# Optimization experiments

Measured on AMD Instinct MI355X. Metric: run time of the kernel, lower is better.

## Reference

```python
import jax, jax.numpy as jnp
import numpy as np

B, S, D, H = 2, 2048, 1024, 16
HD = D // H


def setup_inputs() -> dict:
    key = jax.random.key(0)
    ks = jax.random.split(key, 9)
    x = jax.random.normal(ks[0], (B, S, D), dtype=jnp.float32)
    scale = 1.0 / np.sqrt(D)
    Wq = jax.random.normal(ks[1], (D, D), dtype=jnp.float32) * scale
    bq = jnp.zeros((D,), dtype=jnp.float32)
    Wk = jax.random.normal(ks[2], (D, D), dtype=jnp.float32) * scale
    bk = jnp.zeros((D,), dtype=jnp.float32)
    Wv = jax.random.normal(ks[3], (D, D), dtype=jnp.float32) * scale
    bv = jnp.zeros((D,), dtype=jnp.float32)
    Wo = jax.random.normal(ks[4], (D, D), dtype=jnp.float32) * scale
    bo = jnp.zeros((D,), dtype=jnp.float32)
    return {"x": x, "Wq": Wq, "bq": bq, "Wk": Wk, "bk": bk,
            "Wv": Wv, "bv": bv, "Wo": Wo, "bo": bo}


def reference(x, Wq, bq, Wk, bk, Wv, bv, Wo, bo):
    b, s, d = x.shape
    h, hd = H, HD
    # torch Linear: y = x @ W.T + b
    q = (x @ Wq.T + bq).reshape(b, s, h, hd).transpose(0, 2, 1, 3)  # (b,h,s,hd)
    k = (x @ Wk.T + bk).reshape(b, s, h, hd).transpose(0, 2, 1, 3)
    v = (x @ Wv.T + bv).reshape(b, s, h, hd).transpose(0, 2, 1, 3)
    scores = jnp.einsum('bhqd,bhkd->bhqk', q, k) / np.sqrt(hd)  # (b,h,s,s)
    # FAITHFUL to source: softmax over dim=1 (head axis), not the key axis.
    attn = jax.nn.softmax(scores, axis=1)
    # dropout is identity at inference
    out = jnp.einsum('bhqk,bhkd->bhqd', attn, v)  # (b,h,s,hd)
    out = out.transpose(0, 2, 1, 3).reshape(b, s, d)
    return out @ Wo.T + bo
```

## Files before the change

### kernel.cpp

```cpp
#include <hip/hip_runtime.h>
#include <hip/hip_bf16.h>
#include <cstdint>
#include <cstddef>


typedef __bf16 bf16x8 __attribute__((ext_vector_type(8)));
typedef __bf16 bf16x4 __attribute__((ext_vector_type(4)));
typedef _Float16 f16x2 __attribute__((ext_vector_type(2)));
typedef _Float16 f16x4 __attribute__((ext_vector_type(4)));
typedef _Float16 f16x8 __attribute__((ext_vector_type(8)));
typedef float floatx4 __attribute__((ext_vector_type(4)));

#define S_LEN 2048
#define DIM 1024
#define NH 16
#define HD 64
#define MTOT 4096
#define C_EXP 0.1803368801111244f

__device__ __forceinline__ float fast_exp2(float x) { return __builtin_amdgcn_exp2f(x); }

__device__ __forceinline__ f16x2 pk_cvt(float a, float b) {
    return __builtin_bit_cast(f16x2, __builtin_amdgcn_cvt_pkrtz(a, b));
}

__device__ __forceinline__ void g2l16(const void* g, void* l) {
    __builtin_amdgcn_global_load_lds(
        (const __attribute__((address_space(1))) void*)g,
        (__attribute__((address_space(3))) void*)l, 16, 0, 0);
}

__global__ void cast_all(const float* __restrict__ x,
                         const float* __restrict__ w0, const float* __restrict__ w1,
                         const float* __restrict__ w2, const float* __restrict__ w3,
                         __bf16* __restrict__ xb,
                         __bf16* __restrict__ o0, __bf16* __restrict__ o1,
                         __bf16* __restrict__ o2, _Float16* __restrict__ o3) {
    int bid = blockIdx.x;
    if (bid < 4096) {
        int i = (bid * 256 + threadIdx.x) * 4;
        float4 v = *(const float4*)&x[i];
        bf16x4 o;
        o.x = (__bf16)v.x; o.y = (__bf16)v.y; o.z = (__bf16)v.z; o.w = (__bf16)v.w;
        *(bf16x4*)&xb[i] = o;
        return;
    }
    bid -= 4096;
    int wi = bid >> 10;
    int i = ((bid & 1023) * 256 + threadIdx.x) * 4;
    if (wi == 3) {
        float4 v = *(const float4*)&w3[i];
        f16x4 o;
        o[0] = (_Float16)v.x; o[1] = (_Float16)v.y; o[2] = (_Float16)v.z; o[3] = (_Float16)v.w;
        *(f16x4*)&o3[i] = o;
        return;
    }
    const float* s = (wi == 0) ? w0 : (wi == 1) ? w1 : w2;
    __bf16* d = (wi == 0) ? o0 : (wi == 1) ? o1 : o2;
    float4 v = *(const float4*)&s[i];
    bf16x4 o;
    o.x = (__bf16)v.x; o.y = (__bf16)v.y; o.z = (__bf16)v.z; o.w = (__bf16)v.w;
    *(bf16x4*)&d[i] = o;
}

__global__ __launch_bounds__(256, 2) void qkv_gemm(const __bf16* __restrict__ A,
                                                   const __bf16* __restrict__ Wq,
                                                   const __bf16* __restrict__ Wk,
                                                   const __bf16* __restrict__ Wv,
                                                   const float* __restrict__ bq,
                                                   const float* __restrict__ bk,
                                                   const float* __restrict__ bv,
                                                   __bf16* __restrict__ Qo,
                                                   __bf16* __restrict__ Ko,
                                                   _Float16* __restrict__ Vt) {
    const int tng = blockIdx.x * 128, tm = blockIdx.y * 128;
    const int wsel = tng >> 10, tn = tng & 1023;
    const __bf16* W = (wsel == 0) ? Wq : (wsel == 1) ? Wk : Wv;
    const float* bias = (wsel == 0) ? bq : (wsel == 1) ? bk : bv;
    __shared__ __bf16 As[128 * 32];
    __shared__ __bf16 Bs[128 * 32];
    const int tid = threadIdx.x, wid = tid >> 6, lane = tid & 63;
    const int l15 = lane & 15, quad = lane >> 4;
    const int wm = (wid >> 1) * 64, wn = (wid & 1) * 64;
    floatx4 acc[4][4] = {};
    for (int k0 = 0; k0 < DIM; k0 += 32) {
        __syncthreads();
#pragma unroll
        for (int i = 0; i < 2; ++i) {
            int slot = i * 256 + tid;
            int r = slot >> 2, c8 = (slot & 3) * 8;
            g2l16(&A[(size_t)(tm + r) * DIM + k0 + c8], &As[slot * 8]);
            g2l16(&W[(size_t)(tn + r) * DIM + k0 + c8], &Bs[slot * 8]);
        }
        __syncthreads();
        bf16x8 af[4], bf[4];
#pragma unroll
        for (int t = 0; t < 4; ++t) {
            af[t] = *(const bf16x8*)&As[(wm + t * 16 + l15) * 32 + quad * 8];
            bf[t] = *(const bf16x8*)&Bs[(wn + t * 16 + l15) * 32 + quad * 8];
        }
#pragma unroll
        for (int im = 0; im < 4; ++im)
#pragma unroll
            for (int in = 0; in < 4; ++in)
                acc[im][in] = __builtin_amdgcn_mfma_f32_16x16x32_bf16(af[im], bf[in], acc[im][in], 0, 0, 0);
    }
    if (wsel < 2) {
        __bf16* O = wsel ? Ko : Qo;
#pragma unroll
        for (int im = 0; im < 4; ++im)
#pragma unroll
            for (int in = 0; in < 4; ++in)
#pragma unroll
                for (int r = 0; r < 4; ++r) {
                    int row = tm + wm + im * 16 + quad * 4 + r;
                    int col = tn + wn + in * 16 + l15;
                    O[(size_t)row * DIM + col] = (__bf16)(acc[im][in][r] + bias[col]);
                }
    } else {
#pragma unroll
        for (int im = 0; im < 4; ++im)
#pragma unroll
            for (int in = 0; in < 4; ++in) {
                int cv = tn + wn + in * 16 + l15;
                int row4 = tm + wm + im * 16 + quad * 4;
                float bv_ = bias[cv];
                f16x4 o;
#pragma unroll
                for (int r = 0; r < 4; ++r) o[r] = (_Float16)(acc[im][in][r] + bv_);
                *(f16x4*)&Vt[(size_t)cv * MTOT + row4] = o;
            }
    }
}

__global__ __launch_bounds__(512, 8) void den8(const __bf16* __restrict__ Q,
                                               const __bf16* __restrict__ Km,
                                               _Float16* __restrict__ rd) {
    const int kt = blockIdx.x * 64, qt = blockIdx.y * 128, b = blockIdx.z;
    __shared__ __bf16 Ks[2][2 * 2 * 64 * 32];
    const int tid = threadIdx.x, wid = tid >> 6, lane = tid & 63;
    const int l15 = lane & 15, quad = lane >> 4;
    const int kswz = ((lane >> 1) & 3) << 3;
    const int wq = wid * 16;
    floatx4 dsum[4] = {};
    const size_t qrow = (size_t)(b * S_LEN + qt + wq + l15) * DIM;
    const size_t kbase = (size_t)(b * S_LEN + kt) * DIM;

#pragma unroll
    for (int i = 0; i < 2; ++i) {
        int slot = i * 512 + tid;
        int hs = slot >> 9, rem = slot & 511;
        int p = rem >> 8, rem2 = rem & 255;
        int r = rem2 >> 2;
        int c8 = (((rem2 & 3) ^ ((rem2 >> 3) & 3)) * 8);
        g2l16(&Km[kbase + (size_t)r * DIM + hs * HD + p * 32 + c8], &Ks[0][slot * 8]);
    }
    for (int hh = 0; hh < 8; ++hh) {
        const int cur = hh & 1, nxt = cur ^ 1;
        __syncthreads();
        bf16x8 af[2][2];
#pragma unroll
        for (int hs = 0; hs < 2; ++hs) {
            af[hs][0] = *(const bf16x8*)&Q[qrow + (hh * 2 + hs) * HD + quad * 8];
            af[hs][1] = *(const bf16x8*)&Q[qrow + (hh * 2 + hs) * HD + 32 + quad * 8];
        }
        if (hh + 1 < 8) {
#pragma unroll
            for (int i = 0; i < 2; ++i) {
                int slot = i * 512 + tid;
                int hs = slot >> 9, rem = slot & 511;
                int p = rem >> 8, rem2 = rem & 255;
                int r = rem2 >> 2;
                int c8 = (((rem2 & 3) ^ ((rem2 >> 3) & 3)) * 8);
                g2l16(&Km[kbase + (size_t)r * DIM + ((hh + 1) * 2 + hs) * HD + p * 32 + c8],
                      &Ks[nxt][slot * 8]);
            }
        }
#pragma unroll
        for (int hs = 0; hs < 2; ++hs) {
#pragma unroll
            for (int n = 0; n < 4; ++n) {
                bf16x8 b0 = *(const bf16x8*)&Ks[cur][hs * 4096 + (n * 16 + l15) * 32 + ((quad * 8) ^ kswz)];
                bf16x8 b1 = *(const bf16x8*)&Ks[cur][hs * 4096 + 2048 + (n * 16 + l15) * 32 + ((quad * 8) ^ kswz)];
                floatx4 acc = {};
                acc = __builtin_amdgcn_mfma_f32_16x16x32_bf16(af[hs][0], b0, acc, 0, 0, 0);
                acc = __builtin_amdgcn_mfma_f32_16x16x32_bf16(af[hs][1], b1, acc, 0, 0, 0);
                floatx4 sc = acc * C_EXP;
                floatx4 e;
#pragma unroll
                for (int r = 0; r < 4; ++r) e[r] = fast_exp2(sc[r]);
                dsum[n] += e;
            }
        }
    }
#pragma unroll
    for (int n = 0; n < 4; ++n)
#pragma unroll
        for (int r = 0; r < 4; ++r) {
            int q = qt + wq + quad * 4 + r;
            int k = kt + n * 16 + l15;
            rd[(size_t)(b * S_LEN + q) * S_LEN + k] = (_Float16)(1.0f / dsum[n][r]);
        }
}

__global__ __launch_bounds__(512, 8) void attn8(const __bf16* __restrict__ Q,
                                                const __bf16* __restrict__ Km,
                                                const _Float16* __restrict__ Vt,
                                                const _Float16* __restrict__ rd,
                                                _Float16* __restrict__ AO1,
                                                _Float16* __restrict__ AO2) {
    const int qt = (blockIdx.x >> 1) * 128, ks = blockIdx.x & 1;
    const int h = blockIdx.y, b = blockIdx.z;
    __shared__ __bf16 Ks[2][2 * 64 * 32];
    __shared__ _Float16 Vts[2][64 * 72];
    const int tid = threadIdx.x, wid = tid >> 6, lane = tid & 63;
    const int l15 = lane & 15, quad = lane >> 4;
    const int kswz = ((lane >> 1) & 3) << 3;
    const int wq = wid * 16;
    const size_t qrow = (size_t)(b * S_LEN + qt + wq + l15) * DIM + h * HD;
    bf16x8 qf0 = *(const bf16x8*)&Q[qrow + quad * 8];
    bf16x8 qf1 = *(const bf16x8*)&Q[qrow + 32 + quad * 8];
    const _Float16* rdrow = &rd[(size_t)(b * S_LEN + qt + wq + l15) * S_LEN];
    floatx4 oacc[4] = {};
    const int kt0 = ks * (S_LEN / 2);
    const size_t kdim = (size_t)b * S_LEN * DIM;
    const int vr = tid >> 3, vc = (tid & 7) * 8;
    const int sp = tid >> 8, srem = tid & 255;
    const int sr = srem >> 2;
    const int sc8 = (((srem & 3) ^ ((srem >> 3) & 3)) * 8);

    {
        f16x8 vtmp = *(const f16x8*)&Vt[(size_t)(h * HD + vr) * MTOT + b * S_LEN + kt0 + vc];
        g2l16(&Km[kdim + (size_t)(kt0 + sr) * DIM + h * HD + sp * 32 + sc8], &Ks[0][tid * 8]);
        *(f16x8*)&Vts[0][vr * 72 + vc] = vtmp;
    }
    for (int it = 0; it < 16; ++it) {
        const int cur = it & 1, nxt = cur ^ 1;
        const int kt = kt0 + it * 64;
        __syncthreads();
        f16x4 rv[4];
#pragma unroll
        for (int mp = 0; mp < 4; ++mp)
            rv[mp] = *(const f16x4*)&rdrow[kt + mp * 16 + quad * 4];
        f16x8 vtmp;
        const bool has_next = (it + 1 < 16);
        if (has_next) {
            const int ktn = kt + 64;
            vtmp = *(const f16x8*)&Vt[(size_t)(h * HD + vr) * MTOT + b * S_LEN + ktn + vc];
            g2l16(&Km[kdim + (size_t)(ktn + sr) * DIM + h * HD + sp * 32 + sc8], &Ks[nxt][tid * 8]);
        }
#pragma unroll
        for (int mp = 0; mp < 4; ++mp) {
            bf16x8 kf0 = *(const bf16x8*)&Ks[cur][(mp * 16 + l15) * 32 + ((quad * 8) ^ kswz)];
            bf16x8 kf1 = *(const bf16x8*)&Ks[cur][2048 + (mp * 16 + l15) * 32 + ((quad * 8) ^ kswz)];
            floatx4 s = {};
            s = __builtin_amdgcn_mfma_f32_16x16x32_bf16(kf0, qf0, s, 0, 0, 0);
            s = __builtin_amdgcn_mfma_f32_16x16x32_bf16(kf1, qf1, s, 0, 0, 0);
            floatx4 sc = s * C_EXP;
            f16x2 p01 = pk_cvt(fast_exp2(sc[0]), fast_exp2(sc[1]));
            f16x2 p23 = pk_cvt(fast_exp2(sc[2]), fast_exp2(sc[3]));
            f16x4 pa = __builtin_shufflevector(p01, p23, 0, 1, 2, 3);
            pa = pa * rv[mp];
#pragma unroll
            for (int n = 0; n < 4; ++n) {
                f16x4 vb = *(const f16x4*)&Vts[cur][(n * 16 + l15) * 72 + mp * 16 + quad * 4];
                oacc[n] = __builtin_amdgcn_mfma_f32_16x16x16f16(pa, vb, oacc[n], 0, 0, 0);
            }
        }
        if (has_next) *(f16x8*)&Vts[nxt][vr * 72 + vc] = vtmp;
    }
    _Float16* AO = ks ? AO2 : AO1;
#pragma unroll
    for (int n = 0; n < 4; ++n)
#pragma unroll
        for (int r = 0; r < 4; ++r) {
            int row = qt + wq + quad * 4 + r;
            int col = h * HD + n * 16 + l15;
            AO[(size_t)(b * S_LEN + row) * DIM + col] = (_Float16)oacc[n][r];
        }
}

__global__ __launch_bounds__(256, 2) void gemm_out2(const _Float16* __restrict__ A1,
                                                    const _Float16* __restrict__ A2,
                                                    const _Float16* __restrict__ Bw,
                                                    const float* __restrict__ bias,
                                                    float* __restrict__ C) {
    const int tm = blockIdx.y * 128, tn = blockIdx.x * 64;
    __shared__ _Float16 As1[2 * 128 * 32];
    __shared__ _Float16 As2[2 * 128 * 32];
    __shared__ _Float16 Bs[2 * 64 * 32];
    const int tid = threadIdx.x, wid = tid >> 6, lane = tid & 63;
    const int l15 = lane & 15, quad = lane >> 4;
    const int wm = (wid >> 1) * 64, wn = (wid & 1) * 32;
    floatx4 acc[4][2] = {};
    for (int k0 = 0; k0 < DIM; k0 += 64) {
        __syncthreads();
#pragma unroll
        for (int i = 0; i < 4; ++i) {
            int slot = i * 256 + tid;
            int p = slot >> 9, rem = slot & 511;
            int r = rem >> 2, c8 = (rem & 3) * 8;
            size_t ga = (size_t)(tm + r) * DIM + k0 + p * 32 + c8;
            g2l16(&A1[ga], &As1[slot * 8]);
            g2l16(&A2[ga], &As2[slot * 8]);
        }
#pragma unroll
        for (int i = 0; i < 2; ++i) {
            int slot = i * 256 + tid;
            int p = slot >> 8, rem = slot & 255;
            int r = rem >> 2, c8 = (rem & 3) * 8;
            g2l16(&Bw[(size_t)(tn + r) * DIM + k0 + p * 32 + c8], &Bs[slot * 8]);
        }
        __syncthreads();
#pragma unroll
        for (int kc = 0; kc < 2; ++kc) {
            f16x8 af[4], bf[2];
#pragma unroll
            for (int t = 0; t < 4; ++t) {
                int off = kc * 4096 + (wm + t * 16 + l15) * 32 + quad * 8;
                f16x8 a1 = *(const f16x8*)&As1[off];
                f16x8 a2 = *(const f16x8*)&As2[off];
                af[t] = a1 + a2;
            }
#pragma unroll
            for (int t = 0; t < 2; ++t)
                bf[t] = *(const f16x8*)&Bs[kc * 2048 + (wn + t * 16 + l15) * 32 + quad * 8];
#pragma unroll
            for (int im = 0; im < 4; ++im)
#pragma unroll
                for (int in = 0; in < 2; ++in)
                    acc[im][in] = __builtin_amdgcn_mfma_f32_16x16x32_f16(af[im], bf[in], acc[im][in], 0, 0, 0);
        }
    }
#pragma unroll
    for (int im = 0; im < 4; ++im)
#pragma unroll
        for (int in = 0; in < 2; ++in)
#pragma unroll
            for (int r = 0; r < 4; ++r) {
                int row = tm + wm + im * 16 + quad * 4 + r;
                int col = tn + wn + in * 16 + l15;
                C[(size_t)row * DIM + col] = acc[im][in][r] + bias[col];
            }
}

extern "C" void kernel_launch(void* const* d_in, const int* in_sizes, int n_in,
                              void* d_out, int out_size, void* d_ws, size_t ws_size,
                              hipStream_t stream) {
    const float* x  = (const float*)d_in[0];
    const float* Wq = (const float*)d_in[1];
    const float* bq = (const float*)d_in[2];
    const float* Wk = (const float*)d_in[3];
    const float* bk = (const float*)d_in[4];
    const float* Wv = (const float*)d_in[5];
    const float* bv = (const float*)d_in[6];
    const float* Wo = (const float*)d_in[7];
    const float* bo = (const float*)d_in[8];
    float* out = (float*)d_out;

    char* ws = (char*)d_ws;
    const size_t MB = 1u << 20;
    __bf16*    xb  = (__bf16*)(ws);
    __bf16*    Wqb = (__bf16*)(ws + 8 * MB);
    __bf16*    Wkb = (__bf16*)(ws + 10 * MB);
    __bf16*    Wvb = (__bf16*)(ws + 12 * MB);
    _Float16*  Wof = (_Float16*)(ws + 14 * MB);
    __bf16*    Qb  = (__bf16*)(ws + 16 * MB);
    __bf16*    Kb  = (__bf16*)(ws + 24 * MB);
    _Float16*  VtH = (_Float16*)(ws + 32 * MB);
    _Float16*  rd  = (_Float16*)(ws + 40 * MB);
    _Float16*  AO1 = (_Float16*)(ws + 56 * MB);
    _Float16*  AO2 = (_Float16*)(ws + 64 * MB);

    cast_all<<<8192, 256, 0, stream>>>(x, Wq, Wk, Wv, Wo, xb, Wqb, Wkb, Wvb, Wof);

    qkv_gemm<<<dim3(24, 32), 256, 0, stream>>>(xb, Wqb, Wkb, Wvb, bq, bk, bv, Qb, Kb, VtH);

    den8<<<dim3(S_LEN / 64, S_LEN / 128, 2), 512, 0, stream>>>(Qb, Kb, rd);

    attn8<<<dim3((S_LEN / 128) * 2, NH, 2), 512, 0, stream>>>(Qb, Kb, VtH, rd, AO1, AO2);

    gemm_out2<<<dim3(DIM / 64, MTOT / 128), 256, 0, stream>>>(AO1, AO2, Wof, bo, out);
}
```

Baseline: 268.6 us.

## Process two heads per attention block to share denominator row loads

Each attention block now handles two adjacent heads, staging K and V tiles for both and reusing the per-query reciprocal-denominator loads across them. This halves global reads of the large denominator matrix and Q/tile setup overhead per head. In exchange the grid shrinks by half, LDS and register use per block double, and launch bounds drop to 4 blocks per CU, reducing occupancy.

```diff
diff --git a/kernel.cpp b/kernel.cpp
--- a/kernel.cpp
+++ b/kernel.cpp
@@ -203,36 +203,52 @@
         }
 }
 
-__global__ __launch_bounds__(512, 8) void attn8(const __bf16* __restrict__ Q,
+__global__ __launch_bounds__(512, 4) void attn8(const __bf16* __restrict__ Q,
                                                 const __bf16* __restrict__ Km,
                                                 const _Float16* __restrict__ Vt,
                                                 const _Float16* __restrict__ rd,
                                                 _Float16* __restrict__ AO1,
                                                 _Float16* __restrict__ AO2) {
     const int qt = (blockIdx.x >> 1) * 128, ks = blockIdx.x & 1;
-    const int h = blockIdx.y, b = blockIdx.z;
-    __shared__ __bf16 Ks[2][2 * 64 * 32];
-    __shared__ _Float16 Vts[2][64 * 72];
+    const int h0 = blockIdx.y * 2, b = blockIdx.z;
+    __shared__ __bf16 Ks[2][2 * 2 * 64 * 32];
+    __shared__ _Float16 Vts[2][2 * 64 * 72];
     const int tid = threadIdx.x, wid = tid >> 6, lane = tid & 63;
     const int l15 = lane & 15, quad = lane >> 4;
     const int kswz = ((lane >> 1) & 3) << 3;
     const int wq = wid * 16;
-    const size_t qrow = (size_t)(b * S_LEN + qt + wq + l15) * DIM + h * HD;
-    bf16x8 qf0 = *(const bf16x8*)&Q[qrow + quad * 8];
-    bf16x8 qf1 = *(const bf16x8*)&Q[qrow + 32 + quad * 8];
+    const size_t qrow = (size_t)(b * S_LEN + qt + wq + l15) * DIM + h0 * HD;
+    bf16x8 qf[2][2];
+    qf[0][0] = *(const bf16x8*)&Q[qrow + quad * 8];
+    qf[0][1] = *(const bf16x8*)&Q[qrow + 32 + quad * 8];
+    qf[1][0] = *(const bf16x8*)&Q[qrow + HD + quad * 8];
+    qf[1][1] = *(const bf16x8*)&Q[qrow + HD + 32 + quad * 8];
     const _Float16* rdrow = &rd[(size_t)(b * S_LEN + qt + wq + l15) * S_LEN];
-    floatx4 oacc[4] = {};
+    floatx4 oacc[2][4] = {};
     const int kt0 = ks * (S_LEN / 2);
     const size_t kdim = (size_t)b * S_LEN * DIM;
     const int vr = tid >> 3, vc = (tid & 7) * 8;
-    const int sp = tid >> 8, srem = tid & 255;
-    const int sr = srem >> 2;
-    const int sc8 = (((srem & 3) ^ ((srem >> 3) & 3)) * 8);
+
+#define STAGE_K(BUF, KT_)                                                            \
+    {                                                                                \
+        _Pragma("unroll")                                                            \
+        for (int i = 0; i < 2; ++i) {                                                \
+            int slot = i * 512 + tid;                                                \
+            int hh = slot >> 9, rem = slot & 511;                                    \
+            int p = rem >> 8, rem2 = rem & 255;                                      \
+            int r = rem2 >> 2;                                                       \
+            int c8 = (((rem2 & 3) ^ ((rem2 >> 3) & 3)) * 8);                         \
+            g2l16(&Km[kdim + (size_t)((KT_) + r) * DIM + (h0 + hh) * HD + p * 32 + c8], \
+                  &Ks[BUF][slot * 8]);                                               \
+        }                                                                            \
+    }
 
     {
-        f16x8 vtmp = *(const f16x8*)&Vt[(size_t)(h * HD + vr) * MTOT + b * S_LEN + kt0 + vc];
-        g2l16(&Km[kdim + (size_t)(kt0 + sr) * DIM + h * HD + sp * 32 + sc8], &Ks[0][tid * 8]);
-        *(f16x8*)&Vts[0][vr * 72 + vc] = vtmp;
+        f16x8 v0 = *(const f16x8*)&Vt[(size_t)(h0 * HD + vr) * MTOT + b * S_LEN + kt0 + vc];
+        f16x8 v1 = *(const f16x8*)&Vt[(size_t)((h0 + 1) * HD + vr) * MTOT + b * S_LEN + kt0 + vc];
+        STAGE_K(0, kt0);
+        *(f16x8*)&Vts[0][vr * 72 + vc] = v0;
+        *(f16x8*)&Vts[0][4608 + vr * 72 + vc] = v1;
     }
     for (int it = 0; it < 16; ++it) {
         const int cur = it & 1, nxt = cur ^ 1;
@@ -242,42 +258,56 @@
 #pragma unroll
         for (int mp = 0; mp < 4; ++mp)
             rv[mp] = *(const f16x4*)&rdrow[kt + mp * 16 + quad * 4];
-        f16x8 vtmp;
+        f16x8 vt0, vt1;
         const bool has_next = (it + 1 < 16);
         if (has_next) {
             const int ktn = kt + 64;
-            vtmp = *(const f16x8*)&Vt[(size_t)(h * HD + vr) * MTOT + b * S_LEN + ktn + vc];
-            g2l16(&Km[kdim + (size_t)(ktn + sr) * DIM + h * HD + sp * 32 + sc8], &Ks[nxt][tid * 8]);
+            vt0 = *(const f16x8*)&Vt[(size_t)(h0 * HD + vr) * MTOT + b * S_LEN + ktn + vc];
+            vt1 = *(const f16x8*)&Vt[(size_t)((h0 + 1) * HD + vr) * MTOT + b * S_LEN + ktn + vc];
+            STAGE_K(nxt, ktn);
         }
 #pragma unroll
         for (int mp = 0; mp < 4; ++mp) {
-            bf16x8 kf0 = *(const bf16x8*)&Ks[cur][(mp * 16 + l15) * 32 + ((quad * 8) ^ kswz)];
-            bf16x8 kf1 = *(const bf16x8*)&Ks[cur][2048 + (mp * 16 + l15) * 32 + ((quad * 8) ^ kswz)];
-            floatx4 s = {};
-            s = __builtin_amdgcn_mfma_f32_16x16x32_bf16(kf0, qf0, s, 0, 0, 0);
-            s = __builtin_amdgcn_mfma_f32_16x16x32_bf16(kf1, qf1, s, 0, 0, 0);
-            floatx4 sc = s * C_EXP;
-            f16x2 p01 = pk_cvt(fast_exp2(sc[0]), fast_exp2(sc[1]));
-            f16x2 p23 = pk_cvt(fast_exp2(sc[2]), fast_exp2(sc[3]));
-            f16x4 pa = __builtin_shufflevector(p01, p23, 0, 1, 2, 3);
-            pa = pa * rv[mp];
-#pragma unroll
-            for (int n = 0; n < 4; ++n) {
-                f16x4 vb = *(const f16x4*)&Vts[cur][(n * 16 + l15) * 72 + mp * 16 + quad * 4];
-                oacc[n] = __builtin_amdgcn_mfma_f32_16x16x16f16(pa, vb, oacc[n], 0, 0, 0);
-            }
-        }
-        if (has_next) *(f16x8*)&Vts[nxt][vr * 72 + vc] = vtmp;
-    }
+            const int krow = (mp * 16 + l15) * 32 + ((quad * 8) ^ kswz);
+            f16x4 pa[2];
+#pragma unroll
+            for (int hh = 0; hh < 2; ++hh) {
+                bf16x8 kf0 = *(const bf16x8*)&Ks[cur][hh * 4096 + krow];
+                bf16x8 kf1 = *(const bf16x8*)&Ks[cur][hh * 4096 + 2048 + krow];
+                floatx4 s = {};
+                s = __builtin_amdgcn_mfma_f32_16x16x32_bf16(kf0, qf[hh][0], s, 0, 0, 0);
+                s = __builtin_amdgcn_mfma_f32_16x16x32_bf16(kf1, qf[hh][1], s, 0, 0, 0);
+                floatx4 sc = s * C_EXP;
+                f16x2 p01 = pk_cvt(fast_exp2(sc[0]), fast_exp2(sc[1]));
+                f16x2 p23 = pk_cvt(fast_exp2(sc[2]), fast_exp2(sc[3]));
+                f16x4 p = __builtin_shufflevector(p01, p23, 0, 1, 2, 3);
+                pa[hh] = p * rv[mp];
+            }
+#pragma unroll
+            for (int hh = 0; hh < 2; ++hh)
+#pragma unroll
+                for (int n = 0; n < 4; ++n) {
+                    f16x4 vb = *(const f16x4*)&Vts[cur][hh * 4608 + (n * 16 + l15) * 72 + mp * 16 + quad * 4];
+                    oacc[hh][n] = __builtin_amdgcn_mfma_f32_16x16x16f16(pa[hh], vb, oacc[hh][n], 0, 0, 0);
+                }
+        }
+        if (has_next) {
+            *(f16x8*)&Vts[nxt][vr * 72 + vc] = vt0;
+            *(f16x8*)&Vts[nxt][4608 + vr * 72 + vc] = vt1;
+        }
+    }
+#undef STAGE_K
     _Float16* AO = ks ? AO2 : AO1;
 #pragma unroll
-    for (int n = 0; n < 4; ++n)
-#pragma unroll
-        for (int r = 0; r < 4; ++r) {
-            int row = qt + wq + quad * 4 + r;
-            int col = h * HD + n * 16 + l15;
-            AO[(size_t)(b * S_LEN + row) * DIM + col] = (_Float16)oacc[n][r];
-        }
+    for (int hh = 0; hh < 2; ++hh)
+#pragma unroll
+        for (int n = 0; n < 4; ++n)
+#pragma unroll
+            for (int r = 0; r < 4; ++r) {
+                int row = qt + wq + quad * 4 + r;
+                int col = (h0 + hh) * HD + n * 16 + l15;
+                AO[(size_t)(b * S_LEN + row) * DIM + col] = (_Float16)oacc[hh][n][r];
+            }
 }
 
 __global__ __launch_bounds__(256, 2) void gemm_out2(const _Float16* __restrict__ A1,
@@ -378,7 +408,7 @@
 
     den8<<<dim3(S_LEN / 64, S_LEN / 128, 2), 512, 0, stream>>>(Qb, Kb, rd);
 
-    attn8<<<dim3((S_LEN / 128) * 2, NH, 2), 512, 0, stream>>>(Qb, Kb, VtH, rd, AO1, AO2);
+    attn8<<<dim3((S_LEN / 128) * 2, NH / 2, 2), 512, 0, stream>>>(Qb, Kb, VtH, rd, AO1, AO2);
 
     gemm_out2<<<dim3(DIM / 64, MTOT / 128), 256, 0, stream>>>(AO1, AO2, Wof, bo, out);
 }
```

Measured after the change: 256.2 us. 1.05x faster.
